# Performance work log

Measured on AMD Instinct MI355X. Metric: run time of the kernel, lower is better.

## Reference

```python
import jax, jax.numpy as jnp
import numpy as np

B, T, D = 32, 4096, 512


def setup_inputs() -> dict:
    key = jax.random.key(0)
    k1, k2, k3 = jax.random.split(key, 3)
    inp = jax.random.normal(k1, (B, T, D), dtype=jnp.float32)
    # lengths in [1, T] so every row has at least one valid position
    lens = jax.random.randint(k2, (B,), 1, T + 1, dtype=jnp.int32)
    # matches nn.init.uniform_(slot_embedding, -1/d_hid, 1/d_hid)
    slot_embedding = jax.random.uniform(k3, (D,), dtype=jnp.float32,
                                        minval=-1.0 / D, maxval=1.0 / D)
    return {"inp": inp, "lens": lens, "slot_embedding": slot_embedding}


def reference(inp, lens, slot_embedding):
    # dropout p=0.0 -> identity (eval semantics)
    # scores[b, t] = <inp[b, t, :], slot_embedding>  -> [B, T]
    scores = jnp.einsum("btd,d->bt", inp, slot_embedding)
    # mask padded positions (t >= lens[b]) with -inf, as the per-sample loop does
    valid = jnp.arange(inp.shape[1], dtype=lens.dtype)[None, :] < lens[:, None]  # [B, T]
    scores = jnp.where(valid, scores, -jnp.inf)
    weights = jax.nn.softmax(scores, axis=1)  # [B, T]
    # context[b, d] = sum_t weights[b, t] * inp[b, t, d]
    context = jnp.einsum("bt,btd->bd", weights, inp)
    return context
```

## Files before the change

kernel.cpp:

```cpp
#include <hip/hip_runtime.h>
#include <math.h>


#define BB 32
#define TT 4096
#define DD 512

__global__ __launch_bounds__(256) void
slot_partial_kernel(const float* __restrict__ inp,
                    const int* __restrict__ lens,
                    const float* __restrict__ slot,
                    float* __restrict__ m_arr,
                    float* __restrict__ l_arr,
                    float* __restrict__ c_arr,
                    int CH, int R, int RW) {
    const int chunk = blockIdx.x;
    const int b     = blockIdx.y;
    const int tid   = threadIdx.x;
    const int wave  = tid >> 6;
    const int lane  = tid & 63;
    const int p     = b * CH + chunk;

    const int len = lens[b];
    const int cs  = chunk * R;
    const int ws_start = cs + wave * RW;
    const int ws_end   = min(ws_start + RW, len);

    const float4 s0 = *reinterpret_cast<const float4*>(slot + lane * 4);
    const float4 s1 = *reinterpret_cast<const float4*>(slot + 256 + lane * 4);

    float  m = -INFINITY;
    float  l = 0.0f;
    float4 c0 = make_float4(0.f, 0.f, 0.f, 0.f);
    float4 c1 = make_float4(0.f, 0.f, 0.f, 0.f);

    const float* bp = inp + (size_t)b * TT * DD;

    if (ws_start < ws_end) {
        float4 a[4][2];
        #pragma unroll
        for (int r = 0; r < 4; ++r) {
            const int t = min(ws_start + r, ws_end - 1);
            const float* rp = bp + (size_t)t * DD + lane * 4;
            a[r][0] = *reinterpret_cast<const float4*>(rp);
            a[r][1] = *reinterpret_cast<const float4*>(rp + 256);
        }
        for (int g = ws_start; g < ws_end; g += 4) {
            const int gn = g + 4;
            float4 n[4][2];
            if (gn < ws_end) {
                #pragma unroll
                for (int r = 0; r < 4; ++r) {
                    const int t = min(gn + r, ws_end - 1);
                    const float* rp = bp + (size_t)t * DD + lane * 4;
                    n[r][0] = *reinterpret_cast<const float4*>(rp);
                    n[r][1] = *reinterpret_cast<const float4*>(rp + 256);
                }
            }
            float sd[4];
            #pragma unroll
            for (int r = 0; r < 4; ++r) {
                sd[r] = a[r][0].x * s0.x + a[r][0].y * s0.y
                      + a[r][0].z * s0.z + a[r][0].w * s0.w
                      + a[r][1].x * s1.x + a[r][1].y * s1.y
                      + a[r][1].z * s1.z + a[r][1].w * s1.w;
            }
            #pragma unroll
            for (int off = 32; off >= 1; off >>= 1) {
                #pragma unroll
                for (int r = 0; r < 4; ++r)
                    sd[r] += __shfl_xor(sd[r], off, 64);
            }
            #pragma unroll
            for (int r = 0; r < 4; ++r)
                if (g + r >= ws_end) sd[r] = -INFINITY;

            const float gmax = fmaxf(fmaxf(sd[0], sd[1]), fmaxf(sd[2], sd[3]));
            if (gmax > m) {
                const float alpha = __expf(m - gmax);
                l *= alpha;
                c0.x *= alpha; c0.y *= alpha; c0.z *= alpha; c0.w *= alpha;
                c1.x *= alpha; c1.y *= alpha; c1.z *= alpha; c1.w *= alpha;
                m = gmax;
            }
            #pragma unroll
            for (int r = 0; r < 4; ++r) {
                const float w = __expf(sd[r] - m);
                l += w;
                c0.x += w * a[r][0].x; c0.y += w * a[r][0].y;
                c0.z += w * a[r][0].z; c0.w += w * a[r][0].w;
                c1.x += w * a[r][1].x; c1.y += w * a[r][1].y;
                c1.z += w * a[r][1].z; c1.w += w * a[r][1].w;
            }
            #pragma unroll
            for (int r = 0; r < 4; ++r) { a[r][0] = n[r][0]; a[r][1] = n[r][1]; }
        }
    }

    __shared__ float sm[4];
    __shared__ float sl[4];
    __shared__ float sc[4][DD];

    if (lane == 0) { sm[wave] = m; sl[wave] = l; }
    *reinterpret_cast<float4*>(&sc[wave][lane * 4])       = c0;
    *reinterpret_cast<float4*>(&sc[wave][256 + lane * 4]) = c1;
    __syncthreads();

    const float M = fmaxf(fmaxf(sm[0], sm[1]), fmaxf(sm[2], sm[3]));
    float aw[4];
    float L = 0.0f;
    #pragma unroll
    for (int w = 0; w < 4; ++w) {
        aw[w] = (sm[w] == -INFINITY) ? 0.0f : __expf(sm[w] - M);
        L += sl[w] * aw[w];
    }

    for (int d = tid; d < DD; d += 256) {
        const float acc = sc[0][d] * aw[0] + sc[1][d] * aw[1]
                        + sc[2][d] * aw[2] + sc[3][d] * aw[3];
        c_arr[(size_t)p * DD + d] = acc;
    }
    if (tid == 0) { m_arr[p] = M; l_arr[p] = L; }
}

__global__ __launch_bounds__(256) void
slot_combine_kernel(const float* __restrict__ m_arr,
                    const float* __restrict__ l_arr,
                    const float* __restrict__ c_arr,
                    float* __restrict__ out,
                    int CH) {
    const int b   = blockIdx.x;
    const int tid = threadIdx.x;

    __shared__ float sAlpha[256];

    float M = -INFINITY;
    for (int j = 0; j < CH; ++j) M = fmaxf(M, m_arr[b * CH + j]);

    if (tid < CH) {
        const float mj = m_arr[b * CH + tid];
        sAlpha[tid] = (mj == -INFINITY) ? 0.0f : __expf(mj - M);
    }
    __syncthreads();

    float L = 0.0f;
    for (int j = 0; j < CH; ++j) L += l_arr[b * CH + j] * sAlpha[j];
    const float invL = 1.0f / L;

    const int d = tid * 2;
    float2 acc = make_float2(0.f, 0.f);
    for (int j = 0; j < CH; ++j) {
        const float2 v = *reinterpret_cast<const float2*>(
            c_arr + ((size_t)b * CH + j) * DD + d);
        acc.x += v.x * sAlpha[j];
        acc.y += v.y * sAlpha[j];
    }
    out[b * DD + d]     = acc.x * invL;
    out[b * DD + d + 1] = acc.y * invL;
}

extern "C" void kernel_launch(void* const* d_in, const int* in_sizes, int n_in,
                              void* d_out, int out_size, void* d_ws, size_t ws_size,
                              hipStream_t stream) {
    const float* inp  = (const float*)d_in[0];
    const int*   lens = (const int*)d_in[1];
    const float* slot = (const float*)d_in[2];
    float* out = (float*)d_out;

    int CH = 64;
    while (CH > 1 && (size_t)BB * CH * (2 + DD) * sizeof(float) > ws_size)
        CH >>= 1;
    const int R  = TT / CH;
    const int RW = R / 4;
    const int P  = BB * CH;

    float* m_arr = (float*)d_ws;
    float* l_arr = m_arr + P;
    float* c_arr = l_arr + P;

    dim3 grid1(CH, BB, 1);
    slot_partial_kernel<<<grid1, 256, 0, stream>>>(inp, lens, slot,
                                                   m_arr, l_arr, c_arr,
                                                   CH, R, RW);
    slot_combine_kernel<<<BB, 256, 0, stream>>>(m_arr, l_arr, c_arr, out, CH);
}
```

Measured before the change: 334.3 us.

## Ping-pong register buffers in partial kernel and streamline combine reduction

The partial kernel's prefetch loop now alternates between two register buffers through lambdas instead of copying the prefetched rows into the working set each iteration. Per-chunk max and sum are packed into one float2 array, and partial context rows are written as float2. The combine kernel computes the max and normalizer with wave shuffles instead of a serial loop in every thread, and unrolls the chunk accumulation into four independent accumulators. The aim is to cut register moves and serial latency; the kernel stays bound by reading the input, so the effect is likely small.

```diff
diff --git a/kernel.cpp b/kernel.cpp
--- a/kernel.cpp
+++ b/kernel.cpp
@@ -10,8 +10,7 @@
 slot_partial_kernel(const float* __restrict__ inp,
                     const int* __restrict__ lens,
                     const float* __restrict__ slot,
-                    float* __restrict__ m_arr,
-                    float* __restrict__ l_arr,
+                    float2* __restrict__ ml_arr,
                     float* __restrict__ c_arr,
                     int CH, int R, int RW) {
     const int chunk = blockIdx.x;
@@ -37,33 +36,26 @@
     const float* bp = inp + (size_t)b * TT * DD;
 
     if (ws_start < ws_end) {
-        float4 a[4][2];
-        #pragma unroll
-        for (int r = 0; r < 4; ++r) {
-            const int t = min(ws_start + r, ws_end - 1);
-            const float* rp = bp + (size_t)t * DD + lane * 4;
-            a[r][0] = *reinterpret_cast<const float4*>(rp);
-            a[r][1] = *reinterpret_cast<const float4*>(rp + 256);
-        }
-        for (int g = ws_start; g < ws_end; g += 4) {
-            const int gn = g + 4;
-            float4 n[4][2];
-            if (gn < ws_end) {
-                #pragma unroll
-                for (int r = 0; r < 4; ++r) {
-                    const int t = min(gn + r, ws_end - 1);
-                    const float* rp = bp + (size_t)t * DD + lane * 4;
-                    n[r][0] = *reinterpret_cast<const float4*>(rp);
-                    n[r][1] = *reinterpret_cast<const float4*>(rp + 256);
-                }
-            }
+        float4 bufA[4][2], bufB[4][2];
+
+        auto LOAD = [&](float4 (&buf)[4][2], int g) {
+            #pragma unroll
+            for (int r = 0; r < 4; ++r) {
+                const int t = min(g + r, ws_end - 1);
+                const float* rp = bp + (size_t)t * DD + lane * 4;
+                buf[r][0] = *reinterpret_cast<const float4*>(rp);
+                buf[r][1] = *reinterpret_cast<const float4*>(rp + 256);
+            }
+        };
+
+        auto PROC = [&](float4 (&buf)[4][2], int g) {
             float sd[4];
             #pragma unroll
             for (int r = 0; r < 4; ++r) {
-                sd[r] = a[r][0].x * s0.x + a[r][0].y * s0.y
-                      + a[r][0].z * s0.z + a[r][0].w * s0.w
-                      + a[r][1].x * s1.x + a[r][1].y * s1.y
-                      + a[r][1].z * s1.z + a[r][1].w * s1.w;
+                sd[r] = buf[r][0].x * s0.x + buf[r][0].y * s0.y
+                      + buf[r][0].z * s0.z + buf[r][0].w * s0.w
+                      + buf[r][1].x * s1.x + buf[r][1].y * s1.y
+                      + buf[r][1].z * s1.z + buf[r][1].w * s1.w;
             }
             #pragma unroll
             for (int off = 32; off >= 1; off >>= 1) {
@@ -87,13 +79,27 @@
             for (int r = 0; r < 4; ++r) {
                 const float w = __expf(sd[r] - m);
                 l += w;
-                c0.x += w * a[r][0].x; c0.y += w * a[r][0].y;
-                c0.z += w * a[r][0].z; c0.w += w * a[r][0].w;
-                c1.x += w * a[r][1].x; c1.y += w * a[r][1].y;
-                c1.z += w * a[r][1].z; c1.w += w * a[r][1].w;
-            }
-            #pragma unroll
-            for (int r = 0; r < 4; ++r) { a[r][0] = n[r][0]; a[r][1] = n[r][1]; }
+                c0.x += w * buf[r][0].x; c0.y += w * buf[r][0].y;
+                c0.z += w * buf[r][0].z; c0.w += w * buf[r][0].w;
+                c1.x += w * buf[r][1].x; c1.y += w * buf[r][1].y;
+                c1.z += w * buf[r][1].z; c1.w += w * buf[r][1].w;
+            }
+        };
+
+        int g = ws_start;
+        LOAD(bufA, g);
+        while (true) {
+            int gn = g + 4;
+            if (gn < ws_end) LOAD(bufB, gn);
+            PROC(bufA, g);
+            if (gn >= ws_end) break;
+            g = gn;
+
+            gn = g + 4;
+            if (gn < ws_end) LOAD(bufA, gn);
+            PROC(bufB, g);
+            if (gn >= ws_end) break;
+            g = gn;
         }
     }
 
@@ -115,48 +121,74 @@
         L += sl[w] * aw[w];
     }
 
-    for (int d = tid; d < DD; d += 256) {
-        const float acc = sc[0][d] * aw[0] + sc[1][d] * aw[1]
-                        + sc[2][d] * aw[2] + sc[3][d] * aw[3];
-        c_arr[(size_t)p * DD + d] = acc;
-    }
-    if (tid == 0) { m_arr[p] = M; l_arr[p] = L; }
+    {
+        const int d = tid * 2;
+        float2 acc;
+        acc.x = sc[0][d]     * aw[0] + sc[1][d]     * aw[1]
+              + sc[2][d]     * aw[2] + sc[3][d]     * aw[3];
+        acc.y = sc[0][d + 1] * aw[0] + sc[1][d + 1] * aw[1]
+              + sc[2][d + 1] * aw[2] + sc[3][d + 1] * aw[3];
+        *reinterpret_cast<float2*>(c_arr + (size_t)p * DD + d) = acc;
+    }
+    if (tid == 0) ml_arr[p] = make_float2(M, L);
 }
 
 __global__ __launch_bounds__(256) void
-slot_combine_kernel(const float* __restrict__ m_arr,
-                    const float* __restrict__ l_arr,
+slot_combine_kernel(const float2* __restrict__ ml_arr,
                     const float* __restrict__ c_arr,
                     float* __restrict__ out,
                     int CH) {
     const int b   = blockIdx.x;
     const int tid = threadIdx.x;
 
-    __shared__ float sAlpha[256];
-
-    float M = -INFINITY;
-    for (int j = 0; j < CH; ++j) M = fmaxf(M, m_arr[b * CH + j]);
-
-    if (tid < CH) {
-        const float mj = m_arr[b * CH + tid];
-        sAlpha[tid] = (mj == -INFINITY) ? 0.0f : __expf(mj - M);
+    __shared__ float sAlpha[64];
+    __shared__ float sInvL;
+
+    if (tid < 64) {
+        float mj = -INFINITY, lj = 0.0f;
+        if (tid < CH) {
+            const float2 v = ml_arr[b * CH + tid];
+            mj = v.x; lj = v.y;
+        }
+        float M = mj;
+        #pragma unroll
+        for (int off = 32; off >= 1; off >>= 1)
+            M = fmaxf(M, __shfl_xor(M, off, 64));
+        const float a = (mj == -INFINITY) ? 0.0f : __expf(mj - M);
+        float Lp = lj * a;
+        #pragma unroll
+        for (int off = 32; off >= 1; off >>= 1)
+            Lp += __shfl_xor(Lp, off, 64);
+        sAlpha[tid] = a;
+        if (tid == 0) sInvL = 1.0f / Lp;
     }
     __syncthreads();
 
-    float L = 0.0f;
-    for (int j = 0; j < CH; ++j) L += l_arr[b * CH + j] * sAlpha[j];
-    const float invL = 1.0f / L;
-
+    const float invL = sInvL;
     const int d = tid * 2;
-    float2 acc = make_float2(0.f, 0.f);
-    for (int j = 0; j < CH; ++j) {
-        const float2 v = *reinterpret_cast<const float2*>(
-            c_arr + ((size_t)b * CH + j) * DD + d);
-        acc.x += v.x * sAlpha[j];
-        acc.y += v.y * sAlpha[j];
-    }
-    out[b * DD + d]     = acc.x * invL;
-    out[b * DD + d + 1] = acc.y * invL;
+    const float* cb = c_arr + (size_t)b * CH * DD + d;
+
+    float2 a0 = make_float2(0.f, 0.f), a1 = make_float2(0.f, 0.f);
+    float2 a2 = make_float2(0.f, 0.f), a3 = make_float2(0.f, 0.f);
+    int j = 0;
+    for (; j + 4 <= CH; j += 4) {
+        const float2 v0 = *reinterpret_cast<const float2*>(cb + (size_t)(j + 0) * DD);
+        const float2 v1 = *reinterpret_cast<const float2*>(cb + (size_t)(j + 1) * DD);
+        const float2 v2 = *reinterpret_cast<const float2*>(cb + (size_t)(j + 2) * DD);
+        const float2 v3 = *reinterpret_cast<const float2*>(cb + (size_t)(j + 3) * DD);
+        a0.x += v0.x * sAlpha[j + 0]; a0.y += v0.y * sAlpha[j + 0];
+        a1.x += v1.x * sAlpha[j + 1]; a1.y += v1.y * sAlpha[j + 1];
+        a2.x += v2.x * sAlpha[j + 2]; a2.y += v2.y * sAlpha[j + 2];
+        a3.x += v3.x * sAlpha[j + 3]; a3.y += v3.y * sAlpha[j + 3];
+    }
+    for (; j < CH; ++j) {
+        const float2 v = *reinterpret_cast<const float2*>(cb + (size_t)j * DD);
+        a0.x += v.x * sAlpha[j]; a0.y += v.y * sAlpha[j];
+    }
+    const float accx = (a0.x + a1.x) + (a2.x + a3.x);
+    const float accy = (a0.y + a1.y) + (a2.y + a3.y);
+    out[b * DD + d]     = accx * invL;
+    out[b * DD + d + 1] = accy * invL;
 }
 
 extern "C" void kernel_launch(void* const* d_in, const int* in_sizes, int n_in,
@@ -174,13 +206,12 @@
     const int RW = R / 4;
     const int P  = BB * CH;
 
-    float* m_arr = (float*)d_ws;
-    float* l_arr = m_arr + P;
-    float* c_arr = l_arr + P;
+    float2* ml_arr = (float2*)d_ws;
+    float*  c_arr  = (float*)(ml_arr + P);
 
     dim3 grid1(CH, BB, 1);
     slot_partial_kernel<<<grid1, 256, 0, stream>>>(inp, lens, slot,
-                                                   m_arr, l_arr, c_arr,
+                                                   ml_arr, c_arr,
                                                    CH, R, RW);
-    slot_combine_kernel<<<BB, 256, 0, stream>>>(m_arr, l_arr, c_arr, out, CH);
+    slot_combine_kernel<<<BB, 256, 0, stream>>>(ml_arr, c_arr, out, CH);
 }
```

Result: no change. 329.1 us (-1.6%).
